# Kernel tuning notes

Hardware: AMD Instinct MI355X
Metric: run time of the kernel (lower is better)

## Reference

```python
import jax, jax.numpy as jnp
import numpy as np

H = 56; W = 56; WS = 7; SS = 3; HEADS = 12; DIM = 384
N = WS * WS; NW = (H // WS) * (W // WS); EPS = 1e-5


def _attn_mask():
    img = np.zeros((H, W), np.float32)
    cnt = 0
    for hs in (slice(0, -WS), slice(-WS, -SS), slice(-SS, None)):
        for ws in (slice(0, -WS), slice(-WS, -SS), slice(-SS, None)):
            img[hs, ws] = cnt
            cnt += 1
    m = img.reshape(H // WS, WS, W // WS, WS).transpose(0, 2, 1, 3).reshape(-1, N)
    d = m[:, None, :] - m[:, :, None]
    return jnp.asarray(np.where(d != 0, -100.0, 0.0).astype(np.float32))


def _rel_coords():
    c = np.stack(np.meshgrid(np.arange(WS), np.arange(WS), indexing='ij')).reshape(2, -1)
    rel = (c[:, :, None] - c[:, None, :]).astype(np.float32)
    rel = np.sign(rel) * np.log1p(np.abs(rel))
    return jnp.asarray(np.stack([rel[0], rel[1]], -1).reshape(-1, 2))


ATTN_MASK = _attn_mask()  # (NW, N, N)
REL = _rel_coords()       # (N*N, 2)


def _ln(x, g, b):
    mu = x.mean(-1, keepdims=True)
    var = ((x - mu) ** 2).mean(-1, keepdims=True)
    return (x - mu) / jnp.sqrt(var + EPS) * g + b


def setup_inputs() -> dict:
    key = jax.random.key(0)
    ks = jax.random.split(key, 8)
    s = 0.02
    B = 32
    return {
        'x': jax.random.normal(ks[0], (B, H * W, DIM), jnp.float32),
        'norm1_g': jnp.ones((DIM,), jnp.float32),
        'norm1_b': jnp.zeros((DIM,), jnp.float32),
        'qkv_w': jax.random.normal(ks[1], (DIM, 3 * DIM), jnp.float32) * s,
        'qkv_b': jnp.zeros((3 * DIM,), jnp.float32),
        'tau': jnp.ones((HEADS,), jnp.float32),
        'proj_w': jax.random.normal(ks[2], (DIM, DIM), jnp.float32) * s,
        'proj_b': jnp.zeros((DIM,), jnp.float32),
        'crpb_w1': jax.random.normal(ks[3], (2, 64), jnp.float32) * s,
        'crpb_b1': jnp.zeros((64,), jnp.float32),
        'crpb_w2': jax.random.normal(ks[4], (64, HEADS), jnp.float32) * s,
        'crpb_b2': jnp.zeros((HEADS,), jnp.float32),
        'norm2_g': jnp.ones((DIM,), jnp.float32),
        'norm2_b': jnp.zeros((DIM,), jnp.float32),
        'mlp_w1': jax.random.normal(ks[5], (DIM, 4 * DIM), jnp.float32) * s,
        'mlp_b1': jnp.zeros((4 * DIM,), jnp.float32),
        'mlp_w2': jax.random.normal(ks[6], (4 * DIM, DIM), jnp.float32) * s,
        'mlp_b2': jnp.zeros((DIM,), jnp.float32),
    }


def reference(x, norm1_g, norm1_b, qkv_w, qkv_b, tau, proj_w, proj_b,
              crpb_w1, crpb_b1, crpb_w2, crpb_b2, norm2_g, norm2_b,
              mlp_w1, mlp_b1, mlp_w2, mlp_b2):
    B = x.shape[0]
    shortcut = x
    h = _ln(x, norm1_g, norm1_b).reshape(B, H, W, DIM)
    # cyclic shift
    h = jnp.roll(h, (-SS, -SS), axis=(1, 2))
    # window partition -> (B*NW, N, DIM)
    xw = h.reshape(B, H // WS, WS, W // WS, WS, DIM).transpose(0, 1, 3, 2, 4, 5).reshape(-1, N, DIM)
    qkv = xw @ qkv_w + qkv_b
    q, k, v = jnp.split(qkv, 3, axis=-1)
    hd = DIM // HEADS
    def to_heads(t):
        return t.reshape(-1, N, HEADS, hd).transpose(0, 2, 1, 3)  # (Bw, heads, N, hd)
    q, k, v = to_heads(q), to_heads(k), to_heads(v)
    q = q / jnp.maximum(jnp.linalg.norm(q, axis=-1, keepdims=True), 1e-12)
    k = k / jnp.maximum(jnp.linalg.norm(k, axis=-1, keepdims=True), 1e-12)
    attn = jnp.einsum('whnd,whmd->whnm', q, k) * tau[None, :, None, None]
    # continuous relative position bias
    bias = jax.nn.relu(REL @ crpb_w1 + crpb_b1) @ crpb_w2 + crpb_b2  # (N*N, heads)
    bias = bias.reshape(N, N, HEADS).transpose(2, 0, 1)
    attn = attn + bias[None]
    attn = attn.reshape(B, NW, HEADS, N, N) + ATTN_MASK[None, :, None]
    attn = jax.nn.softmax(attn.reshape(-1, HEADS, N, N), axis=-1)
    out = jnp.einsum('whnm,whmd->whnd', attn, v).transpose(0, 2, 1, 3).reshape(-1, N, DIM)
    out = out @ proj_w + proj_b
    # window reverse
    h = out.reshape(B, H // WS, W // WS, WS, WS, DIM).transpose(0, 1, 3, 2, 4, 5).reshape(B, H, W, DIM)
    h = jnp.roll(h, (SS, SS), axis=(1, 2)).reshape(B, H * W, DIM)
    x = shortcut + h
    m = _ln(x, norm2_g, norm2_b)
    m = jax.nn.gelu(m @ mlp_w1 + mlp_b1, approximate=False) @ mlp_w2 + mlp_b2
    return x + m
```

## Files before the change

kernel.cpp:

```cpp
#include <hip/hip_runtime.h>
#include <cstdint>
#include <cstddef>


#ifndef AB_TWOHALF
#define AB_TWOHALF 0
#endif

typedef unsigned short u16;
typedef __bf16 bf16x8 __attribute__((ext_vector_type(8)));
typedef __bf16 bf16x4 __attribute__((ext_vector_type(4)));
typedef float f32x4 __attribute__((ext_vector_type(4)));

__device__ __forceinline__ u16 f2bf(float f) {
  unsigned u = __builtin_bit_cast(unsigned, f);
  u += 0x7fffu + ((u >> 16) & 1u);
  return (u16)(u >> 16);
}

__device__ __forceinline__ bf16x8 ldfrag(const u16* rowp, int l4) {
#if AB_TWOHALF
  bf16x4 lo = *(const bf16x4*)(rowp + 4 * l4);
  bf16x4 hi = *(const bf16x4*)(rowp + 16 + 4 * l4);
  bf16x8 r;
  r[0]=lo[0]; r[1]=lo[1]; r[2]=lo[2]; r[3]=lo[3];
  r[4]=hi[0]; r[5]=hi[1]; r[6]=hi[2]; r[7]=hi[3];
  return r;
#else
  return *(const bf16x8*)(rowp + 8 * l4);
#endif
}

__global__ __launch_bounds__(256) void fill_k(float* o, int n) {
  int i = blockIdx.x * 256 + threadIdx.x;
  if (i < n) o[i] = 12345.0f;
}

__global__ __launch_bounds__(256) void wconv_k(
    const float* __restrict__ qkv_w, const float* __restrict__ proj_w,
    const float* __restrict__ mlp_w1, const float* __restrict__ mlp_w2,
    u16* __restrict__ o) {
  const int id = blockIdx.x * 256 + threadIdx.x;
  if (id < 442368) {
    const int n = id / 384, k = id - n * 384;
    o[id] = f2bf(qkv_w[k * 1152 + n]);
  } else if (id < 589824) {
    const int e = id - 442368; const int n = e / 384, k = e - n * 384;
    o[id] = f2bf(proj_w[k * 384 + n]);
  } else if (id < 1179648) {
    const int e = id - 589824; const int n = e / 384, k = e - n * 384;
    o[id] = f2bf(mlp_w1[k * 1536 + n]);
  } else {
    const int e = id - 1179648; const int n = e / 1536, k = e - n * 1536;
    o[id] = f2bf(mlp_w2[k * 384 + n]);
  }
}

__global__ __launch_bounds__(256) void biastab_k(
    const float* __restrict__ w1, const float* __restrict__ b1,
    const float* __restrict__ w2, const float* __restrict__ b2,
    float* __restrict__ biasT) {
  const int id = blockIdx.x * 256 + threadIdx.x;
  if (id >= 2401) return;
  const int i = id / 49, j = id - i * 49;
  const int r1 = i / 7, c1 = i - r1 * 7, r2 = j / 7, c2 = j - r2 * 7;
  float dy = (float)(r1 - r2), dx = (float)(c1 - c2);
  dy = copysignf(log1pf(fabsf(dy)), dy);
  dx = copysignf(log1pf(fabsf(dx)), dx);
  float accv[12];
#pragma unroll
  for (int t = 0; t < 12; ++t) accv[t] = b2[t];
  for (int u = 0; u < 64; ++u) {
    float hu = fmaxf(dy * w1[u] + dx * w1[64 + u] + b1[u], 0.0f);
#pragma unroll
    for (int t = 0; t < 12; ++t) accv[t] += hu * w2[u * 12 + t];
  }
#pragma unroll
  for (int t = 0; t < 12; ++t) biasT[t * 2401 + id] = accv[t];
}

template <int WINMAP>
__global__ __launch_bounds__(256, 4) void ln_k(
    const float* __restrict__ X, const float* __restrict__ g,
    const float* __restrict__ b, u16* __restrict__ O) {
  const int t = blockIdx.x * 4 + (threadIdx.x >> 6);
  const int lane = threadIdx.x & 63;
  const float* xr = X + (size_t)t * 384;
  float v[6];
  float s = 0.f;
#pragma unroll
  for (int i = 0; i < 6; ++i) { v[i] = xr[lane + i * 64]; s += v[i]; }
#pragma unroll
  for (int m = 1; m < 64; m <<= 1) s += __shfl_xor(s, m);
  const float mu = s * (1.0f / 384.0f);
  float q = 0.f;
#pragma unroll
  for (int i = 0; i < 6; ++i) { float d = v[i] - mu; q += d * d; }
#pragma unroll
  for (int m = 1; m < 64; m <<= 1) q += __shfl_xor(q, m);
  const float rstd = rsqrtf(q * (1.0f / 384.0f) + 1e-5f);
  size_t row;
  if constexpr (WINMAP) {
    const int bb = t / 3136, hw = t - bb * 3136;
    const int ho = hw / 56, wo = hw - ho * 56;
    int hs = ho - 3; if (hs < 0) hs += 56;
    int ws2 = wo - 3; if (ws2 < 0) ws2 += 56;
    const int h7 = hs / 7, w7 = ws2 / 7;
    const int wwin = bb * 64 + h7 * 8 + w7;
    const int p = (hs - h7 * 7) * 7 + (ws2 - w7 * 7);
    row = (size_t)wwin * 49 + p;
  } else {
    row = (size_t)t;
  }
  u16* orow = O + row * 384;
#pragma unroll
  for (int i = 0; i < 6; ++i) {
    const int d = lane + i * 64;
    orow[d] = f2bf((v[i] - mu) * rstd * g[d] + b[d]);
  }
}

template <int EPI>
__global__ __launch_bounds__(256, 2) void gemm_k(
    const u16* __restrict__ A, const u16* __restrict__ Bt,
    const float* __restrict__ bias, const float* __restrict__ aux,
    void* __restrict__ outp, int M, int N, int K) {
  __shared__ u16 Ash[128 * 32];
  __shared__ u16 Bsh[128 * 32];
  const int tid = threadIdx.x;
  const int lane = tid & 63;
  const int wid = tid >> 6;
  const int wrow = wid >> 1, wcol = wid & 1;
  const int l15 = lane & 15, l4 = lane >> 4;
  const int tileM = blockIdx.y * 128;
  const int tileN = blockIdx.x * 128;

  f32x4 acc[4][4] = {};

  const int srow = tid >> 2;
  const int scol = (tid & 3) * 8;

  for (int k0 = 0; k0 < K; k0 += 32) {
    uint4 a0 = *(const uint4*)(A + (size_t)(tileM + srow) * K + k0 + scol);
    uint4 a1 = *(const uint4*)(A + (size_t)(tileM + 64 + srow) * K + k0 + scol);
    uint4 b0 = *(const uint4*)(Bt + (size_t)(tileN + srow) * K + k0 + scol);
    uint4 b1 = *(const uint4*)(Bt + (size_t)(tileN + 64 + srow) * K + k0 + scol);
    __syncthreads();
    *(uint4*)&Ash[srow * 32 + scol] = a0;
    *(uint4*)&Ash[(64 + srow) * 32 + scol] = a1;
    *(uint4*)&Bsh[srow * 32 + scol] = b0;
    *(uint4*)&Bsh[(64 + srow) * 32 + scol] = b1;
    __syncthreads();
    bf16x8 af[4], bfr[4];
#pragma unroll
    for (int f = 0; f < 4; ++f) {
      af[f] = ldfrag(&Ash[(wrow * 64 + f * 16 + l15) * 32], l4);
      bfr[f] = ldfrag(&Bsh[(wcol * 64 + f * 16 + l15) * 32], l4);
    }
#pragma unroll
    for (int fm = 0; fm < 4; ++fm)
#pragma unroll
      for (int fn = 0; fn < 4; ++fn)
        acc[fm][fn] = __builtin_amdgcn_mfma_f32_16x16x32_bf16(
            af[fm], bfr[fn], acc[fm][fn], 0, 0, 0);
  }

  const int baseRow = tileM + wrow * 64;
  const int baseCol = tileN + wcol * 64;

  if constexpr (EPI == 0) {
    u16* O = (u16*)outp;
#pragma unroll
    for (int fm = 0; fm < 4; ++fm) {
#pragma unroll
      for (int hp = 0; hp < 2; ++hp) {
        const int c0 = baseCol + hp * 32;
        const int seg = c0 >> 5;
        const bool nrm = seg < 24;
        const float tfac = (seg < 12) ? aux[seg] : 1.0f;
        const float b0 = bias[c0 + l15];
        const float b1 = bias[c0 + 16 + l15];
#pragma unroll
        for (int r = 0; r < 4; ++r) {
          float v0 = acc[fm][2 * hp][r] + b0;
          float v1 = acc[fm][2 * hp + 1][r] + b1;
          if (nrm) {
            float ss = v0 * v0 + v1 * v1;
            ss += __shfl_xor(ss, 1);
            ss += __shfl_xor(ss, 2);
            ss += __shfl_xor(ss, 4);
            ss += __shfl_xor(ss, 8);
            const float f = tfac / fmaxf(sqrtf(ss), 1e-12f);
            v0 *= f; v1 *= f;
          }
          const size_t row = (size_t)(baseRow + fm * 16 + l4 * 4 + r);
          O[row * N + c0 + l15] = f2bf(v0);
          O[row * N + c0 + 16 + l15] = f2bf(v1);
        }
      }
    }
  } else if constexpr (EPI == 1) {
    float* O = (float*)outp;
    const float* X = aux;
#pragma unroll
    for (int fm = 0; fm < 4; ++fm) {
#pragma unroll
      for (int r = 0; r < 4; ++r) {
        const int row = baseRow + fm * 16 + l4 * 4 + r;
        const int w = row / 49, p = row - w * 49;
        const int bb = w >> 6, widx = w & 63;
        const int p7 = p / 7;
        int hs = (widx >> 3) * 7 + p7;
        int ws2 = (widx & 7) * 7 + (p - p7 * 7);
        int ho = hs + 3; if (ho >= 56) ho -= 56;
        int wo = ws2 + 3; if (wo >= 56) wo -= 56;
        const size_t tok = (size_t)bb * 3136 + ho * 56 + wo;
#pragma unroll
        for (int fn = 0; fn < 4; ++fn) {
          const int col = baseCol + fn * 16 + l15;
          O[tok * 384 + col] = X[tok * 384 + col] + acc[fm][fn][r] + bias[col];
        }
      }
    }
  } else if constexpr (EPI == 2) {
    u16* O = (u16*)outp;
#pragma unroll
    for (int fm = 0; fm < 4; ++fm) {
#pragma unroll
      for (int fn = 0; fn < 4; ++fn) {
        const int col = baseCol + fn * 16 + l15;
        const float bc = bias[col];
#pragma unroll
        for (int r = 0; r < 4; ++r) {
          const size_t row = (size_t)(baseRow + fm * 16 + l4 * 4 + r);
          const float v = acc[fm][fn][r] + bc;
          const float g = 0.5f * v * (1.0f + erff(v * 0.70710678118654752f));
          O[row * N + col] = f2bf(g);
        }
      }
    }
  } else {
    float* O = (float*)outp;
#pragma unroll
    for (int fm = 0; fm < 4; ++fm) {
#pragma unroll
      for (int fn = 0; fn < 4; ++fn) {
        const int col = baseCol + fn * 16 + l15;
        const float bc = bias[col];
#pragma unroll
        for (int r = 0; r < 4; ++r) {
          const size_t row = (size_t)(baseRow + fm * 16 + l4 * 4 + r);
          O[row * N + col] += acc[fm][fn][r] + bc;
        }
      }
    }
  }
}

__global__ __launch_bounds__(256, 2) void attn_k(
    const u16* __restrict__ qkv, const float* __restrict__ biasT,
    u16* __restrict__ outp) {
  __shared__ u16 lds[4][7552];
  const int tid = threadIdx.x, lane = tid & 63, wid = tid >> 6;
  const int l15 = lane & 15, l4 = lane >> 4;
  const int W = blockIdx.x * 4 + wid;
  const int w = W / 12, h = W - w * 12;
  u16* S = lds[wid];
  u16* Q = S;
  u16* Kl = S + 2560;
  u16* P = S;
  u16* VT = S + 5120;
  float* sums = (float*)(S + 7424);
  const u16* base = qkv + (size_t)w * 56448 + h * 32;
  const int widx = w & 63, wh = widx >> 3, ww = widx & 7;
  const bool masked = (wh == 7) || (ww == 7);

#pragma unroll
  for (int it = 0; it < 4; ++it) {
    const int row = it * 16 + (lane >> 2);
    const int c8 = (lane & 3) * 8;
    uint4 qv = {0, 0, 0, 0}, kv = {0, 0, 0, 0};
    if (row < 49) {
      qv = *(const uint4*)(base + (size_t)row * 1152 + c8);
      kv = *(const uint4*)(base + (size_t)row * 1152 + 384 + c8);
    }
    *(uint4*)&Q[row * 40 + c8] = qv;
    *(uint4*)&Kl[row * 40 + c8] = kv;
  }
  {
    const int d = lane & 31;
    const int jh = lane >> 5;
#pragma unroll 4
    for (int jt = 0; jt < 32; ++jt) {
      const int j = jt * 2 + jh;
      u16 val = 0;
      if (j < 49) val = base[(size_t)j * 1152 + 768 + d];
      VT[d * 72 + j] = val;
    }
  }
  __syncthreads();

  f32x4 sc[4][4] = {};
  {
    bf16x8 aq[4], bk[4];
#pragma unroll
    for (int f = 0; f < 4; ++f) aq[f] = ldfrag(&Q[(f * 16 + l15) * 40], l4);
#pragma unroll
    for (int f = 0; f < 4; ++f) bk[f] = ldfrag(&Kl[(f * 16 + l15) * 40], l4);
#pragma unroll
    for (int fm = 0; fm < 4; ++fm)
#pragma unroll
      for (int fn = 0; fn < 4; ++fn)
        sc[fm][fn] = __builtin_amdgcn_mfma_f32_16x16x32_bf16(
            aq[fm], bk[fn], sc[fm][fn], 0, 0, 0);
  }
  __syncthreads();

  int codej[4] = {0, 0, 0, 0};
  if (masked) {
#pragma unroll
    for (int fn = 0; fn < 4; ++fn) {
      const int j = fn * 16 + l15;
      const int pr = j / 7, pc = j - pr * 7;
      const int rr2 = (wh == 7) ? ((pr < 4) ? 1 : 2) : 0;
      const int cc2 = (ww == 7) ? ((pc < 4) ? 1 : 2) : 0;
      codej[fn] = rr2 * 3 + cc2;
    }
  }
#pragma unroll
  for (int fm = 0; fm < 4; ++fm) {
#pragma unroll
    for (int r = 0; r < 4; ++r) {
      const int i = fm * 16 + l4 * 4 + r;
      const bool iok = i < 49;
      int ci = 0;
      if (masked && iok) {
        const int pr = i / 7, pc = i - pr * 7;
        const int rr2 = (wh == 7) ? ((pr < 4) ? 1 : 2) : 0;
        const int cc2 = (ww == 7) ? ((pc < 4) ? 1 : 2) : 0;
        ci = rr2 * 3 + cc2;
      }
      const float* brow = biasT + (size_t)h * 2401 + (iok ? i : 0) * 49;
      float sv[4];
#pragma unroll
      for (int fn = 0; fn < 4; ++fn) {
        const int j = fn * 16 + l15;
        float s = sc[fm][fn][r];
        if (iok && j < 49) {
          s += brow[j];
          if (masked && codej[fn] != ci) s -= 100.0f;
        } else {
          s = -1e30f;
        }
        sv[fn] = s;
      }
      float mx = fmaxf(fmaxf(sv[0], sv[1]), fmaxf(sv[2], sv[3]));
      mx = fmaxf(mx, __shfl_xor(mx, 1));
      mx = fmaxf(mx, __shfl_xor(mx, 2));
      mx = fmaxf(mx, __shfl_xor(mx, 4));
      mx = fmaxf(mx, __shfl_xor(mx, 8));
      float sm = 0.f;
      u16 pb[4];
#pragma unroll
      for (int fn = 0; fn < 4; ++fn) {
        const float e = __expf(sv[fn] - mx);
        sm += e;
        pb[fn] = f2bf(e);
      }
      sm += __shfl_xor(sm, 1);
      sm += __shfl_xor(sm, 2);
      sm += __shfl_xor(sm, 4);
      sm += __shfl_xor(sm, 8);
#pragma unroll
      for (int fn = 0; fn < 4; ++fn) P[i * 72 + fn * 16 + l15] = pb[fn];
      if (l15 == 0) sums[i] = sm;
    }
  }
  __syncthreads();

  f32x4 o[4][2] = {};
#pragma unroll
  for (int kk = 0; kk < 2; ++kk) {
    bf16x8 pa[4], bv[2];
#pragma unroll
    for (int fm = 0; fm < 4; ++fm)
      pa[fm] = ldfrag(&P[(fm * 16 + l15) * 72 + kk * 32], l4);
#pragma unroll
    for (int fn = 0; fn < 2; ++fn)
      bv[fn] = ldfrag(&VT[(fn * 16 + l15) * 72 + kk * 32], l4);
#pragma unroll
    for (int fm = 0; fm < 4; ++fm)
#pragma unroll
      for (int fn = 0; fn < 2; ++fn)
        o[fm][fn] = __builtin_amdgcn_mfma_f32_16x16x32_bf16(
            pa[fm], bv[fn], o[fm][fn], 0, 0, 0);
  }
  u16* ob = outp + (size_t)w * 49 * 384 + h * 32;
#pragma unroll
  for (int fm = 0; fm < 4; ++fm) {
#pragma unroll
    for (int r = 0; r < 4; ++r) {
      const int i = fm * 16 + l4 * 4 + r;
      if (i < 49) {
        const float inv = 1.0f / sums[i];
        ob[(size_t)i * 384 + l15] = f2bf(o[fm][0][r] * inv);
        ob[(size_t)i * 384 + 16 + l15] = f2bf(o[fm][1][r] * inv);
      }
    }
  }
}

extern "C" void kernel_launch(void* const* d_in, const int* in_sizes, int n_in,
                              void* d_out, int out_size, void* d_ws,
                              size_t ws_size, hipStream_t stream) {
  const float* x      = (const float*)d_in[0];
  const float* n1g    = (const float*)d_in[1];
  const float* n1b    = (const float*)d_in[2];
  const float* qkv_w  = (const float*)d_in[3];
  const float* qkv_b  = (const float*)d_in[4];
  const float* tau    = (const float*)d_in[5];
  const float* proj_w = (const float*)d_in[6];
  const float* proj_b = (const float*)d_in[7];
  const float* c_w1   = (const float*)d_in[8];
  const float* c_b1   = (const float*)d_in[9];
  const float* c_w2   = (const float*)d_in[10];
  const float* c_b2   = (const float*)d_in[11];
  const float* n2g    = (const float*)d_in[12];
  const float* n2b    = (const float*)d_in[13];
  const float* mlp_w1 = (const float*)d_in[14];
  const float* mlp_b1 = (const float*)d_in[15];
  const float* mlp_w2 = (const float*)d_in[16];
  const float* mlp_b2 = (const float*)d_in[17];
  float* out = (float*)d_out;
  char* ws = (char*)d_ws;

  constexpr size_t WS_WT    = 0;
  constexpr size_t WS_BIAST = 3538944;
  constexpr size_t WS_XW    = 4194304;
  constexpr size_t WS_QKV   = 81264640;
  constexpr size_t WS_ATT   = 312475648;
  constexpr size_t WS_NEED  = 389545984;

  if (ws_size < WS_NEED) {
    fill_k<<<(out_size + 255) / 256, 256, 0, stream>>>(out, out_size);
    return;
  }

  u16* wqkvT  = (u16*)(ws + WS_WT);
  u16* wprojT = (u16*)(ws + WS_WT + 884736);
  u16* wm1T   = (u16*)(ws + WS_WT + 1179648);
  u16* wm2T   = (u16*)(ws + WS_WT + 2359296);
  float* biasT = (float*)(ws + WS_BIAST);
  u16* xw  = (u16*)(ws + WS_XW);
  u16* qkv = (u16*)(ws + WS_QKV);
  u16* att = (u16*)(ws + WS_ATT);
  u16* hid = qkv;
  u16* ln2 = xw;

  wconv_k<<<6912, 256, 0, stream>>>(qkv_w, proj_w, mlp_w1, mlp_w2, (u16*)ws);
  biastab_k<<<10, 256, 0, stream>>>(c_w1, c_b1, c_w2, c_b2, biasT);
  ln_k<1><<<25088, 256, 0, stream>>>(x, n1g, n1b, xw);
  gemm_k<0><<<dim3(9, 784), 256, 0, stream>>>(xw, wqkvT, qkv_b, tau, qkv,
                                              100352, 1152, 384);
  attn_k<<<6144, 256, 0, stream>>>(qkv, biasT, att);
  gemm_k<1><<<dim3(3, 784), 256, 0, stream>>>(att, wprojT, proj_b, x, out,
                                              100352, 384, 384);
  ln_k<0><<<25088, 256, 0, stream>>>(out, n2g, n2b, ln2);
  gemm_k<2><<<dim3(12, 784), 256, 0, stream>>>(ln2, wm1T, mlp_b1, nullptr, hid,
                                               100352, 1536, 384);
  gemm_k<3><<<dim3(3, 784), 256, 0, stream>>>(hid, wm2T, mlp_b2, nullptr, out,
                                              100352, 384, 1536);
}
```

Baseline: 1.446 ms.

## Load GEMM tiles directly into LDS and remap workgroups across XCDs

The GEMM main loop now stages A and B tiles with global_load_lds, writing global data straight into shared memory instead of going through registers first. It also permutes the linear block id so that consecutive tiles are spread across the eight XCDs, which is meant to improve L2 reuse. This cuts VGPR pressure and store instructions, but the loop still has no double-buffering, so load latency is still exposed at each barrier. The remap assumes the block count is divisible by eight, and the LDS layout is assumed to match the per-lane 16-byte write order.

Result: faster. 1.383 ms (-4.3%).

```diff
diff --git a/kernel.cpp b/kernel.cpp
--- a/kernel.cpp
+++ b/kernel.cpp
@@ -3,13 +3,8 @@
 #include <cstddef>
 
 
-#ifndef AB_TWOHALF
-#define AB_TWOHALF 0
-#endif
-
 typedef unsigned short u16;
 typedef __bf16 bf16x8 __attribute__((ext_vector_type(8)));
-typedef __bf16 bf16x4 __attribute__((ext_vector_type(4)));
 typedef float f32x4 __attribute__((ext_vector_type(4)));
 
 __device__ __forceinline__ u16 f2bf(float f) {
@@ -18,17 +13,14 @@
   return (u16)(u >> 16);
 }
 
+__device__ __forceinline__ void gll16(const u16* g, u16* l) {
+  __builtin_amdgcn_global_load_lds(
+      (const __attribute__((address_space(1))) void*)g,
+      (__attribute__((address_space(3))) void*)l, 16, 0, 0);
+}
+
 __device__ __forceinline__ bf16x8 ldfrag(const u16* rowp, int l4) {
-#if AB_TWOHALF
-  bf16x4 lo = *(const bf16x4*)(rowp + 4 * l4);
-  bf16x4 hi = *(const bf16x4*)(rowp + 16 + 4 * l4);
-  bf16x8 r;
-  r[0]=lo[0]; r[1]=lo[1]; r[2]=lo[2]; r[3]=lo[3];
-  r[4]=hi[0]; r[5]=hi[1]; r[6]=hi[2]; r[7]=hi[3];
-  return r;
-#else
   return *(const bf16x8*)(rowp + 8 * l4);
-#endif
 }
 
 __global__ __launch_bounds__(256) void fill_k(float* o, int n) {
@@ -129,27 +121,35 @@
   __shared__ u16 Bsh[128 * 32];
   const int tid = threadIdx.x;
   const int lane = tid & 63;
-  const int wid = tid >> 6;
-  const int wrow = wid >> 1, wcol = wid & 1;
+  const int wv = tid >> 6;
+  const int wrow = wv >> 1, wcol = wv & 1;
   const int l15 = lane & 15, l4 = lane >> 4;
-  const int tileM = blockIdx.y * 128;
-  const int tileN = blockIdx.x * 128;
+
+  const int nx = gridDim.x;
+  const int nwg = nx * gridDim.y;
+  int bid = blockIdx.y * nx + blockIdx.x;
+  bid = (bid & 7) * (nwg >> 3) + (bid >> 3);
+  const int tileN = (bid % nx) * 128;
+  const int tileM = (bid / nx) * 128;
 
   f32x4 acc[4][4] = {};
 
-  const int srow = tid >> 2;
-  const int scol = (tid & 3) * 8;
+  const int r0 = wv * 16 + (lane >> 2);
+  const int c0 = (lane & 3) * 8;
+  const u16* Ag = A + (size_t)(tileM + r0) * K + c0;
+  const u16* Bg = Bt + (size_t)(tileN + r0) * K + c0;
+  const size_t rowskip = (size_t)64 * K;
+  u16* Al0 = &Ash[wv * 512];
+  u16* Al1 = &Ash[(4 + wv) * 512];
+  u16* Bl0 = &Bsh[wv * 512];
+  u16* Bl1 = &Bsh[(4 + wv) * 512];
 
   for (int k0 = 0; k0 < K; k0 += 32) {
-    uint4 a0 = *(const uint4*)(A + (size_t)(tileM + srow) * K + k0 + scol);
-    uint4 a1 = *(const uint4*)(A + (size_t)(tileM + 64 + srow) * K + k0 + scol);
-    uint4 b0 = *(const uint4*)(Bt + (size_t)(tileN + srow) * K + k0 + scol);
-    uint4 b1 = *(const uint4*)(Bt + (size_t)(tileN + 64 + srow) * K + k0 + scol);
     __syncthreads();
-    *(uint4*)&Ash[srow * 32 + scol] = a0;
-    *(uint4*)&Ash[(64 + srow) * 32 + scol] = a1;
-    *(uint4*)&Bsh[srow * 32 + scol] = b0;
-    *(uint4*)&Bsh[(64 + srow) * 32 + scol] = b1;
+    gll16(Ag + k0, Al0);
+    gll16(Ag + rowskip + k0, Al1);
+    gll16(Bg + k0, Bl0);
+    gll16(Bg + rowskip + k0, Bl1);
     __syncthreads();
     bf16x8 af[4], bfr[4];
 #pragma unroll
@@ -174,12 +174,12 @@
     for (int fm = 0; fm < 4; ++fm) {
 #pragma unroll
       for (int hp = 0; hp < 2; ++hp) {
-        const int c0 = baseCol + hp * 32;
-        const int seg = c0 >> 5;
+        const int c0e = baseCol + hp * 32;
+        const int seg = c0e >> 5;
         const bool nrm = seg < 24;
         const float tfac = (seg < 12) ? aux[seg] : 1.0f;
-        const float b0 = bias[c0 + l15];
-        const float b1 = bias[c0 + 16 + l15];
+        const float b0 = bias[c0e + l15];
+        const float b1 = bias[c0e + 16 + l15];
 #pragma unroll
         for (int r = 0; r < 4; ++r) {
           float v0 = acc[fm][2 * hp][r] + b0;
@@ -194,8 +194,8 @@
             v0 *= f; v1 *= f;
           }
           const size_t row = (size_t)(baseRow + fm * 16 + l4 * 4 + r);
-          O[row * N + c0 + l15] = f2bf(v0);
-          O[row * N + c0 + 16 + l15] = f2bf(v1);
+          O[row * N + c0e + l15] = f2bf(v0);
+          O[row * N + c0e + 16 + l15] = f2bf(v1);
         }
       }
     }
```
